# Kernel tuning notes

Hardware: AMD Instinct MI355X
Metric: run time of the kernel (lower is better)

## Reference

```python
import jax, jax.numpy as jnp
import numpy as np

B, N, D_IN, D_OUT = 16, 4096, 256, 128


def setup_inputs() -> dict:
    key = jax.random.key(0)
    ks = jax.random.split(key, 7)
    s_proj = float(np.sqrt(2.0 / D_IN))   # kaiming-ish scale
    s_mlp = float(np.sqrt(2.0 / D_OUT))
    return {
        "X": jax.random.normal(ks[0], (B, N, D_IN), dtype=jnp.float32),
        "W_proj": jax.random.normal(ks[1], (D_IN, D_OUT), dtype=jnp.float32) * s_proj,
        "b_proj": jnp.zeros((D_OUT,), dtype=jnp.float32),
        "W1": jax.random.normal(ks[2], (D_OUT, D_OUT), dtype=jnp.float32) * s_mlp,
        "b1": jnp.zeros((D_OUT,), dtype=jnp.float32),
        "W2": jax.random.normal(ks[3], (D_OUT, D_OUT), dtype=jnp.float32) * s_mlp,
        "b2": jnp.zeros((D_OUT,), dtype=jnp.float32),
    }


def reference(X, W_proj, b_proj, W1, b1, W2, b2):
    # proj: Linear(input_dim, output_dim)
    X = jnp.einsum("bnd,de->bne", X, W_proj) + b_proj
    # mlp: FeedForwardNetwork(D,D,D, num_layers=2) == Linear -> ReLU -> Linear
    X = jax.nn.relu(jnp.einsum("bnd,de->bne", X, W1) + b1)
    X = jnp.einsum("bnd,de->bne", X, W2) + b2
    # leave-one-out sum over the N axis: for each row i, sum of all rows j != i.
    # Identical math to the masked (B,N,N,D) expand-reduce in the torch source.
    return X.sum(axis=1, keepdims=True) - X
```

## Files before the change

kernel.cpp:

```cpp
#include <hip/hip_runtime.h>
#include <stdint.h>

#define D_IN  256
#define D_OUT 128
#define NSEQ  4096
#define NB    16
#define TILE_M 64
#define GRID_M ((NB * NSEQ) / TILE_M)
#define LDS_BYTES 32768

typedef __bf16 bf16x8 __attribute__((ext_vector_type(8)));
typedef float  f32x4  __attribute__((ext_vector_type(4)));

__device__ __forceinline__ unsigned short f2bf(float f) {
  __bf16 h = (__bf16)f;
  union { __bf16 h; unsigned short u; } c; c.h = h;
  return c.u;
}
__device__ __forceinline__ float bf2f(unsigned short u) {
  union { unsigned int u; float f; } a; a.u = ((unsigned int)u) << 16;
  return a.f;
}

__global__ __launch_bounds__(256) void prep(
    const float* __restrict__ Wp, const float* __restrict__ W1, const float* __restrict__ W2,
    const float* __restrict__ bp, const float* __restrict__ b1,
    unsigned short* __restrict__ WaT, unsigned short* __restrict__ W2T, float* __restrict__ be1) {
  int b = blockIdx.x;
  if (b < 128) {
    __shared__ float wp[256];
    int k0 = b * 2;
    wp[threadIdx.x] = Wp[k0 * 128 + threadIdx.x];
    __syncthreads();
    int kk = threadIdx.x >> 7, n = threadIdx.x & 127;
    float s = 0.f;
#pragma unroll 16
    for (int j = 0; j < 128; ++j) s += wp[kk * 128 + j] * W1[j * 128 + n];
    WaT[n * 256 + (k0 + kk)] = f2bf(s);
  } else if (b < 192) {
    int t = (b - 128) * 256 + threadIdx.x;
    int k = t >> 7, n = t & 127;
    W2T[n * 128 + k] = f2bf(W2[t]);
  } else {
    if (threadIdx.x < 128) {
      int n = threadIdx.x;
      float s = b1[n];
#pragma unroll 16
      for (int j = 0; j < 128; ++j) s += bp[j] * W1[j * 128 + n];
      be1[n] = s;
    }
  }
}

template <bool USE_WS>
__global__ __launch_bounds__(256, 3) void fused2(
    const float* __restrict__ X,
    const unsigned short* __restrict__ WaT,
    const unsigned short* __restrict__ W2T,
    const float* __restrict__ be1, const float* __restrict__ b2v,
    unsigned short* __restrict__ Y3, float* __restrict__ out, float* __restrict__ P) {
  extern __shared__ unsigned short smem[];
  unsigned short* bufA = smem;
  unsigned short* bufB = smem + 8192;

  const int tid  = threadIdx.x;
  const int lane = tid & 63;
  const int w    = tid >> 6;
  const int q    = lane >> 4;
  const int l16  = lane & 15;
  const int rowbase = blockIdx.x * TILE_M;
  const int col0 = w * 32 + l16;
  const int col1 = col0 + 16;

  f32x4 acc[4][2];
  bf16x8 bA[4][2], bB[4][2];

#pragma unroll
  for (int ks = 0; ks < 4; ++ks) {
    bA[ks][0] = *(const bf16x8*)(WaT + (size_t)col0 * 256 + ks * 32 + q * 8);
    bA[ks][1] = *(const bf16x8*)(WaT + (size_t)col1 * 256 + ks * 32 + q * 8);
  }

#pragma unroll
  for (int it = 0; it < 8; ++it) {
    int i = tid + it * 256;
    int r = i >> 5, c4 = (i & 31) << 2;
    const float4 v = *(const float4*)(X + (size_t)(rowbase + r) * D_IN + c4);
    ushort4 u; u.x = f2bf(v.x); u.y = f2bf(v.y); u.z = f2bf(v.z); u.w = f2bf(v.w);
    *(ushort4*)(bufA + r * 128 + ((((c4 >> 3) ^ (r & 15)) << 3) + (c4 & 7))) = u;
  }

#pragma unroll
  for (int rt = 0; rt < 4; ++rt) {
    acc[rt][0] = (f32x4){0.f, 0.f, 0.f, 0.f};
    acc[rt][1] = (f32x4){0.f, 0.f, 0.f, 0.f};
  }
  __syncthreads();

  float4 xv[8];
#pragma unroll
  for (int it = 0; it < 8; ++it) {
    int i = tid + it * 256;
    int r = i >> 5, c4 = (i & 31) << 2;
    xv[it] = *(const float4*)(X + (size_t)(rowbase + r) * D_IN + 128 + c4);
  }
#pragma unroll
  for (int ks = 0; ks < 4; ++ks) {
    bB[ks][0] = *(const bf16x8*)(WaT + (size_t)col0 * 256 + 128 + ks * 32 + q * 8);
    bB[ks][1] = *(const bf16x8*)(WaT + (size_t)col1 * 256 + 128 + ks * 32 + q * 8);
  }

#pragma unroll
  for (int ks = 0; ks < 4; ++ks)
#pragma unroll
    for (int rt = 0; rt < 4; ++rt) {
      bf16x8 a = *(const bf16x8*)(bufA + (rt * 16 + l16) * 128 + (((4 * ks + q) ^ l16) << 3));
      acc[rt][0] = __builtin_amdgcn_mfma_f32_16x16x32_bf16(a, bA[ks][0], acc[rt][0], 0, 0, 0);
      acc[rt][1] = __builtin_amdgcn_mfma_f32_16x16x32_bf16(a, bA[ks][1], acc[rt][1], 0, 0, 0);
    }

#pragma unroll
  for (int it = 0; it < 8; ++it) {
    int i = tid + it * 256;
    int r = i >> 5, c4 = (i & 31) << 2;
    ushort4 u; u.x = f2bf(xv[it].x); u.y = f2bf(xv[it].y); u.z = f2bf(xv[it].z); u.w = f2bf(xv[it].w);
    *(ushort4*)(bufB + r * 128 + ((((c4 >> 3) ^ (r & 15)) << 3) + (c4 & 7))) = u;
  }
  __syncthreads();

#pragma unroll
  for (int ks = 0; ks < 4; ++ks) {
    bA[ks][0] = *(const bf16x8*)(W2T + (size_t)col0 * 128 + ks * 32 + q * 8);
    bA[ks][1] = *(const bf16x8*)(W2T + (size_t)col1 * 128 + ks * 32 + q * 8);
  }

#pragma unroll
  for (int ks = 0; ks < 4; ++ks)
#pragma unroll
    for (int rt = 0; rt < 4; ++rt) {
      bf16x8 a = *(const bf16x8*)(bufB + (rt * 16 + l16) * 128 + (((4 * ks + q) ^ l16) << 3));
      acc[rt][0] = __builtin_amdgcn_mfma_f32_16x16x32_bf16(a, bB[ks][0], acc[rt][0], 0, 0, 0);
      acc[rt][1] = __builtin_amdgcn_mfma_f32_16x16x32_bf16(a, bB[ks][1], acc[rt][1], 0, 0, 0);
    }

  {
    const float e0 = be1[col0], e1 = be1[col1];
#pragma unroll
    for (int rt = 0; rt < 4; ++rt)
#pragma unroll
      for (int r = 0; r < 4; ++r) {
        int row = rt * 16 + q * 4 + r;
        int sw = (row & 15) << 3;
        float v0 = acc[rt][0][r] + e0; v0 = v0 > 0.f ? v0 : 0.f;
        float v1 = acc[rt][1][r] + e1; v1 = v1 > 0.f ? v1 : 0.f;
        bufA[row * 128 + ((((col0 >> 3) << 3) ^ sw) + (col0 & 7))] = f2bf(v0);
        bufA[row * 128 + ((((col1 >> 3) << 3) ^ sw) + (col1 & 7))] = f2bf(v1);
      }
  }
  __syncthreads();

#pragma unroll
  for (int rt = 0; rt < 4; ++rt) {
    acc[rt][0] = (f32x4){0.f, 0.f, 0.f, 0.f};
    acc[rt][1] = (f32x4){0.f, 0.f, 0.f, 0.f};
  }
#pragma unroll
  for (int ks = 0; ks < 4; ++ks)
#pragma unroll
    for (int rt = 0; rt < 4; ++rt) {
      bf16x8 a = *(const bf16x8*)(bufA + (rt * 16 + l16) * 128 + (((4 * ks + q) ^ l16) << 3));
      acc[rt][0] = __builtin_amdgcn_mfma_f32_16x16x32_bf16(a, bA[ks][0], acc[rt][0], 0, 0, 0);
      acc[rt][1] = __builtin_amdgcn_mfma_f32_16x16x32_bf16(a, bA[ks][1], acc[rt][1], 0, 0, 0);
    }

  {
    const float bb0 = b2v[col0], bb1 = b2v[col1];
    float s0 = 0.f, s1 = 0.f;
#pragma unroll
    for (int rt = 0; rt < 4; ++rt)
#pragma unroll
      for (int r = 0; r < 4; ++r) {
        int row = rt * 16 + q * 4 + r;
        int sw = (row & 15) << 3;
        float v0 = acc[rt][0][r] + bb0;
        float v1 = acc[rt][1][r] + bb1;
        s0 += v0; s1 += v1;
        bufB[row * 128 + ((((col0 >> 3) << 3) ^ sw) + (col0 & 7))] = f2bf(v0);
        bufB[row * 128 + ((((col1 >> 3) << 3) ^ sw) + (col1 & 7))] = f2bf(v1);
      }
    s0 += __shfl_down(s0, 16); s0 += __shfl_down(s0, 32);
    s1 += __shfl_down(s1, 16); s1 += __shfl_down(s1, 32);
    if (lane < 16) {
      P[(size_t)blockIdx.x * 128 + col0] = s0;
      P[(size_t)blockIdx.x * 128 + col1] = s1;
    }
  }
  __syncthreads();

  if (USE_WS) {
#pragma unroll
    for (int it = 0; it < 4; ++it) {
      int i = tid + it * 256;
      int r = i >> 4, g = i & 15;
      *(uint4*)(Y3 + (size_t)(rowbase + r) * 128 + g * 8) =
          *(const uint4*)(bufB + r * 128 + ((g ^ (r & 15)) << 3));
    }
  } else {
#pragma unroll
    for (int it = 0; it < 8; ++it) {
      int i = tid + it * 256;
      int r = i >> 5, c4 = (i & 31) << 2;
      ushort4 u = *(const ushort4*)(bufB + r * 128 + ((((c4 >> 3) ^ (r & 15)) << 3) + (c4 & 7)));
      float4 v; v.x = bf2f(u.x); v.y = bf2f(u.y); v.z = bf2f(u.z); v.w = bf2f(u.w);
      *(float4*)(out + (size_t)(rowbase + r) * D_OUT + c4) = v;
    }
  }
}

__global__ __launch_bounds__(256) void reduce_S(const float* __restrict__ P, float* __restrict__ S) {
  __shared__ float tmp[128];
  int b = blockIdx.x;
  int col = threadIdx.x & 127;
  int h = threadIdx.x >> 7;
  float s = 0.f;
#pragma unroll
  for (int i = 0; i < 32; ++i) s += P[(size_t)(b * 64 + h * 32 + i) * 128 + col];
  if (h == 1) tmp[col] = s;
  __syncthreads();
  if (h == 0) S[b * 128 + col] = s + tmp[col];
}

__global__ __launch_bounds__(256) void finalize_ws(
    float* __restrict__ out, const unsigned short* __restrict__ Y3, const float* __restrict__ S) {
  size_t g = (size_t)blockIdx.x * 256 + threadIdx.x;
  size_t base = g * 8;
  int row = (int)(base >> 7);
  int col = (int)(base & 127);
  int b = row >> 12;
  uint4 u = *(const uint4*)(Y3 + base);
  float4 s0 = *(const float4*)(S + (b << 7) + col);
  float4 s1 = *(const float4*)(S + (b << 7) + col + 4);
  union { unsigned int uu; float f; } t;
  float4 o0, o1;
  t.uu = u.x << 16;          o0.x = s0.x - t.f;
  t.uu = u.x & 0xFFFF0000u;  o0.y = s0.y - t.f;
  t.uu = u.y << 16;          o0.z = s0.z - t.f;
  t.uu = u.y & 0xFFFF0000u;  o0.w = s0.w - t.f;
  t.uu = u.z << 16;          o1.x = s1.x - t.f;
  t.uu = u.z & 0xFFFF0000u;  o1.y = s1.y - t.f;
  t.uu = u.w << 16;          o1.z = s1.z - t.f;
  t.uu = u.w & 0xFFFF0000u;  o1.w = s1.w - t.f;
  *(float4*)(out + base) = o0;
  *(float4*)(out + base + 4) = o1;
}

__global__ __launch_bounds__(256) void finalize_ip(float* __restrict__ out, const float* __restrict__ S) {
  size_t g = (size_t)blockIdx.x * 256 + threadIdx.x;
  size_t base = g * 8;
  int row = (int)(base >> 7);
  int col = (int)(base & 127);
  int b = row >> 12;
  float4 s0 = *(const float4*)(S + (b << 7) + col);
  float4 s1 = *(const float4*)(S + (b << 7) + col + 4);
  float4 y0 = *(const float4*)(out + base);
  float4 y1 = *(const float4*)(out + base + 4);
  float4 o0, o1;
  o0.x = s0.x - y0.x; o0.y = s0.y - y0.y; o0.z = s0.z - y0.z; o0.w = s0.w - y0.w;
  o1.x = s1.x - y1.x; o1.y = s1.y - y1.y; o1.z = s1.z - y1.z; o1.w = s1.w - y1.w;
  *(float4*)(out + base) = o0;
  *(float4*)(out + base + 4) = o1;
}

extern "C" void kernel_launch(void* const* d_in, const int* in_sizes, int n_in,
                              void* d_out, int out_size, void* d_ws, size_t ws_size,
                              hipStream_t stream) {
  const float* X  = (const float*)d_in[0];
  const float* Wp = (const float*)d_in[1];
  const float* bp = (const float*)d_in[2];
  const float* W1 = (const float*)d_in[3];
  const float* b1 = (const float*)d_in[4];
  const float* W2 = (const float*)d_in[5];
  const float* b2 = (const float*)d_in[6];
  float* out = (float*)d_out;

  char* ws = (char*)d_ws;
  float* S            = (float*)ws;
  float* be1          = (float*)(ws + 8192);
  unsigned short* WaT = (unsigned short*)(ws + 12288);
  unsigned short* W2T = (unsigned short*)(ws + 12288 + 65536);
  float* P            = (float*)(ws + 12288 + 65536 + 32768);
  unsigned short* Y3  = (unsigned short*)(ws + 12288 + 65536 + 32768 + 524288);

  const size_t need = 12288 + 65536 + 32768 + 524288 + (size_t)NB * NSEQ * D_OUT * 2;
  const bool use_ws = ws_size >= need;

  prep<<<193, 256, 0, stream>>>(Wp, W1, W2, bp, b1, WaT, W2T, be1);

  const int fin_blocks = (NB * NSEQ * D_OUT) / (8 * 256);
  if (use_ws) {
    fused2<true><<<GRID_M, 256, LDS_BYTES, stream>>>(X, WaT, W2T, be1, b2, Y3, out, P);
    reduce_S<<<NB, 256, 0, stream>>>(P, S);
    finalize_ws<<<fin_blocks, 256, 0, stream>>>(out, Y3, S);
  } else {
    fused2<false><<<GRID_M, 256, LDS_BYTES, stream>>>(X, WaT, W2T, be1, b2, Y3, out, P);
    reduce_S<<<NB, 256, 0, stream>>>(P, S);
    finalize_ip<<<fin_blocks, 256, 0, stream>>>(out, S);
  }
}
```

Before: 134.3 us.

## Process two row tiles per block and fold S reduction into finalize

The fused kernel now runs 512 blocks that each loop over two 64-row tiles, accumulating the column partial sums across both tiles, which halves the partial-sum buffer. The separate reduce_S launch is removed; each finalize block instead recomputes its batch's column sums from 32 partials into shared memory. This cuts one kernel launch and its dependency gap, at the cost of redundant small reductions in every finalize block and fewer, longer blocks in the main kernel (512 blocks may underfill the GPU's CUs).

```diff
diff --git a/kernel.cpp b/kernel.cpp
--- a/kernel.cpp
+++ b/kernel.cpp
@@ -5,8 +5,7 @@
 #define D_OUT 128
 #define NSEQ  4096
 #define NB    16
-#define TILE_M 64
-#define GRID_M ((NB * NSEQ) / TILE_M)
+#define NBLK  512
 #define LDS_BYTES 32768
 
 typedef __bf16 bf16x8 __attribute__((ext_vector_type(8)));
@@ -68,83 +67,89 @@
   const int w    = tid >> 6;
   const int q    = lane >> 4;
   const int l16  = lane & 15;
-  const int rowbase = blockIdx.x * TILE_M;
+  const int blk  = blockIdx.x;
   const int col0 = w * 32 + l16;
   const int col1 = col0 + 16;
 
+  const float e0  = be1[col0], e1  = be1[col1];
+  const float bb0 = b2v[col0], bb1 = b2v[col1];
+
   f32x4 acc[4][2];
   bf16x8 bA[4][2], bB[4][2];
-
-#pragma unroll
-  for (int ks = 0; ks < 4; ++ks) {
-    bA[ks][0] = *(const bf16x8*)(WaT + (size_t)col0 * 256 + ks * 32 + q * 8);
-    bA[ks][1] = *(const bf16x8*)(WaT + (size_t)col1 * 256 + ks * 32 + q * 8);
-  }
-
-#pragma unroll
-  for (int it = 0; it < 8; ++it) {
-    int i = tid + it * 256;
-    int r = i >> 5, c4 = (i & 31) << 2;
-    const float4 v = *(const float4*)(X + (size_t)(rowbase + r) * D_IN + c4);
-    ushort4 u; u.x = f2bf(v.x); u.y = f2bf(v.y); u.z = f2bf(v.z); u.w = f2bf(v.w);
-    *(ushort4*)(bufA + r * 128 + ((((c4 >> 3) ^ (r & 15)) << 3) + (c4 & 7))) = u;
-  }
-
-#pragma unroll
-  for (int rt = 0; rt < 4; ++rt) {
-    acc[rt][0] = (f32x4){0.f, 0.f, 0.f, 0.f};
-    acc[rt][1] = (f32x4){0.f, 0.f, 0.f, 0.f};
-  }
-  __syncthreads();
-
-  float4 xv[8];
-#pragma unroll
-  for (int it = 0; it < 8; ++it) {
-    int i = tid + it * 256;
-    int r = i >> 5, c4 = (i & 31) << 2;
-    xv[it] = *(const float4*)(X + (size_t)(rowbase + r) * D_IN + 128 + c4);
-  }
-#pragma unroll
-  for (int ks = 0; ks < 4; ++ks) {
-    bB[ks][0] = *(const bf16x8*)(WaT + (size_t)col0 * 256 + 128 + ks * 32 + q * 8);
-    bB[ks][1] = *(const bf16x8*)(WaT + (size_t)col1 * 256 + 128 + ks * 32 + q * 8);
-  }
-
-#pragma unroll
-  for (int ks = 0; ks < 4; ++ks)
+  float s0 = 0.f, s1 = 0.f;
+
+#pragma unroll 1
+  for (int t = 0; t < 2; ++t) {
+    const int rowbase = blk * 128 + t * 64;
+
+#pragma unroll
+    for (int ks = 0; ks < 4; ++ks) {
+      bA[ks][0] = *(const bf16x8*)(WaT + (size_t)col0 * 256 + ks * 32 + q * 8);
+      bA[ks][1] = *(const bf16x8*)(WaT + (size_t)col1 * 256 + ks * 32 + q * 8);
+    }
+
+#pragma unroll
+    for (int it = 0; it < 8; ++it) {
+      int i = tid + it * 256;
+      int r = i >> 5, c4 = (i & 31) << 2;
+      const float4 v = *(const float4*)(X + (size_t)(rowbase + r) * D_IN + c4);
+      ushort4 u; u.x = f2bf(v.x); u.y = f2bf(v.y); u.z = f2bf(v.z); u.w = f2bf(v.w);
+      *(ushort4*)(bufA + r * 128 + ((((c4 >> 3) ^ (r & 15)) << 3) + (c4 & 7))) = u;
+    }
+
 #pragma unroll
     for (int rt = 0; rt < 4; ++rt) {
-      bf16x8 a = *(const bf16x8*)(bufA + (rt * 16 + l16) * 128 + (((4 * ks + q) ^ l16) << 3));
-      acc[rt][0] = __builtin_amdgcn_mfma_f32_16x16x32_bf16(a, bA[ks][0], acc[rt][0], 0, 0, 0);
-      acc[rt][1] = __builtin_amdgcn_mfma_f32_16x16x32_bf16(a, bA[ks][1], acc[rt][1], 0, 0, 0);
-    }
-
-#pragma unroll
-  for (int it = 0; it < 8; ++it) {
-    int i = tid + it * 256;
-    int r = i >> 5, c4 = (i & 31) << 2;
-    ushort4 u; u.x = f2bf(xv[it].x); u.y = f2bf(xv[it].y); u.z = f2bf(xv[it].z); u.w = f2bf(xv[it].w);
-    *(ushort4*)(bufB + r * 128 + ((((c4 >> 3) ^ (r & 15)) << 3) + (c4 & 7))) = u;
-  }
-  __syncthreads();
-
-#pragma unroll
-  for (int ks = 0; ks < 4; ++ks) {
-    bA[ks][0] = *(const bf16x8*)(W2T + (size_t)col0 * 128 + ks * 32 + q * 8);
-    bA[ks][1] = *(const bf16x8*)(W2T + (size_t)col1 * 128 + ks * 32 + q * 8);
-  }
-
-#pragma unroll
-  for (int ks = 0; ks < 4; ++ks)
-#pragma unroll
-    for (int rt = 0; rt < 4; ++rt) {
-      bf16x8 a = *(const bf16x8*)(bufB + (rt * 16 + l16) * 128 + (((4 * ks + q) ^ l16) << 3));
-      acc[rt][0] = __builtin_amdgcn_mfma_f32_16x16x32_bf16(a, bB[ks][0], acc[rt][0], 0, 0, 0);
-      acc[rt][1] = __builtin_amdgcn_mfma_f32_16x16x32_bf16(a, bB[ks][1], acc[rt][1], 0, 0, 0);
-    }
-
-  {
-    const float e0 = be1[col0], e1 = be1[col1];
+      acc[rt][0] = (f32x4){0.f, 0.f, 0.f, 0.f};
+      acc[rt][1] = (f32x4){0.f, 0.f, 0.f, 0.f};
+    }
+    __syncthreads();
+
+    float4 xv[8];
+#pragma unroll
+    for (int it = 0; it < 8; ++it) {
+      int i = tid + it * 256;
+      int r = i >> 5, c4 = (i & 31) << 2;
+      xv[it] = *(const float4*)(X + (size_t)(rowbase + r) * D_IN + 128 + c4);
+    }
+#pragma unroll
+    for (int ks = 0; ks < 4; ++ks) {
+      bB[ks][0] = *(const bf16x8*)(WaT + (size_t)col0 * 256 + 128 + ks * 32 + q * 8);
+      bB[ks][1] = *(const bf16x8*)(WaT + (size_t)col1 * 256 + 128 + ks * 32 + q * 8);
+    }
+
+#pragma unroll
+    for (int ks = 0; ks < 4; ++ks)
+#pragma unroll
+      for (int rt = 0; rt < 4; ++rt) {
+        bf16x8 a = *(const bf16x8*)(bufA + (rt * 16 + l16) * 128 + (((4 * ks + q) ^ l16) << 3));
+        acc[rt][0] = __builtin_amdgcn_mfma_f32_16x16x32_bf16(a, bA[ks][0], acc[rt][0], 0, 0, 0);
+        acc[rt][1] = __builtin_amdgcn_mfma_f32_16x16x32_bf16(a, bA[ks][1], acc[rt][1], 0, 0, 0);
+      }
+
+#pragma unroll
+    for (int it = 0; it < 8; ++it) {
+      int i = tid + it * 256;
+      int r = i >> 5, c4 = (i & 31) << 2;
+      ushort4 u; u.x = f2bf(xv[it].x); u.y = f2bf(xv[it].y); u.z = f2bf(xv[it].z); u.w = f2bf(xv[it].w);
+      *(ushort4*)(bufB + r * 128 + ((((c4 >> 3) ^ (r & 15)) << 3) + (c4 & 7))) = u;
+    }
+    __syncthreads();
+
+#pragma unroll
+    for (int ks = 0; ks < 4; ++ks) {
+      bA[ks][0] = *(const bf16x8*)(W2T + (size_t)col0 * 128 + ks * 32 + q * 8);
+      bA[ks][1] = *(const bf16x8*)(W2T + (size_t)col1 * 128 + ks * 32 + q * 8);
+    }
+
+#pragma unroll
+    for (int ks = 0; ks < 4; ++ks)
+#pragma unroll
+      for (int rt = 0; rt < 4; ++rt) {
+        bf16x8 a = *(const bf16x8*)(bufB + (rt * 16 + l16) * 128 + (((4 * ks + q) ^ l16) << 3));
+        acc[rt][0] = __builtin_amdgcn_mfma_f32_16x16x32_bf16(a, bB[ks][0], acc[rt][0], 0, 0, 0);
+        acc[rt][1] = __builtin_amdgcn_mfma_f32_16x16x32_bf16(a, bB[ks][1], acc[rt][1], 0, 0, 0);
+      }
+
 #pragma unroll
     for (int rt = 0; rt < 4; ++rt)
 #pragma unroll
@@ -156,26 +161,22 @@
         bufA[row * 128 + ((((col0 >> 3) << 3) ^ sw) + (col0 & 7))] = f2bf(v0);
         bufA[row * 128 + ((((col1 >> 3) << 3) ^ sw) + (col1 & 7))] = f2bf(v1);
       }
-  }
-  __syncthreads();
-
-#pragma unroll
-  for (int rt = 0; rt < 4; ++rt) {
-    acc[rt][0] = (f32x4){0.f, 0.f, 0.f, 0.f};
-    acc[rt][1] = (f32x4){0.f, 0.f, 0.f, 0.f};
-  }
-#pragma unroll
-  for (int ks = 0; ks < 4; ++ks)
+    __syncthreads();
+
 #pragma unroll
     for (int rt = 0; rt < 4; ++rt) {
-      bf16x8 a = *(const bf16x8*)(bufA + (rt * 16 + l16) * 128 + (((4 * ks + q) ^ l16) << 3));
-      acc[rt][0] = __builtin_amdgcn_mfma_f32_16x16x32_bf16(a, bA[ks][0], acc[rt][0], 0, 0, 0);
-      acc[rt][1] = __builtin_amdgcn_mfma_f32_16x16x32_bf16(a, bA[ks][1], acc[rt][1], 0, 0, 0);
-    }
-
-  {
-    const float bb0 = b2v[col0], bb1 = b2v[col1];
-    float s0 = 0.f, s1 = 0.f;
+      acc[rt][0] = (f32x4){0.f, 0.f, 0.f, 0.f};
+      acc[rt][1] = (f32x4){0.f, 0.f, 0.f, 0.f};
+    }
+#pragma unroll
+    for (int ks = 0; ks < 4; ++ks)
+#pragma unroll
+      for (int rt = 0; rt < 4; ++rt) {
+        bf16x8 a = *(const bf16x8*)(bufA + (rt * 16 + l16) * 128 + (((4 * ks + q) ^ l16) << 3));
+        acc[rt][0] = __builtin_amdgcn_mfma_f32_16x16x32_bf16(a, bA[ks][0], acc[rt][0], 0, 0, 0);
+        acc[rt][1] = __builtin_amdgcn_mfma_f32_16x16x32_bf16(a, bA[ks][1], acc[rt][1], 0, 0, 0);
+      }
+
 #pragma unroll
     for (int rt = 0; rt < 4; ++rt)
 #pragma unroll
@@ -188,58 +189,55 @@
         bufB[row * 128 + ((((col0 >> 3) << 3) ^ sw) + (col0 & 7))] = f2bf(v0);
         bufB[row * 128 + ((((col1 >> 3) << 3) ^ sw) + (col1 & 7))] = f2bf(v1);
       }
-    s0 += __shfl_down(s0, 16); s0 += __shfl_down(s0, 32);
-    s1 += __shfl_down(s1, 16); s1 += __shfl_down(s1, 32);
-    if (lane < 16) {
-      P[(size_t)blockIdx.x * 128 + col0] = s0;
-      P[(size_t)blockIdx.x * 128 + col1] = s1;
-    }
+    __syncthreads();
+
+    if (USE_WS) {
+#pragma unroll
+      for (int it = 0; it < 4; ++it) {
+        int i = tid + it * 256;
+        int r = i >> 4, g = i & 15;
+        *(uint4*)(Y3 + (size_t)(rowbase + r) * 128 + g * 8) =
+            *(const uint4*)(bufB + r * 128 + ((g ^ (r & 15)) << 3));
+      }
+    } else {
+#pragma unroll
+      for (int it = 0; it < 8; ++it) {
+        int i = tid + it * 256;
+        int r = i >> 5, c4 = (i & 31) << 2;
+        ushort4 u = *(const ushort4*)(bufB + r * 128 + ((((c4 >> 3) ^ (r & 15)) << 3) + (c4 & 7)));
+        float4 v; v.x = bf2f(u.x); v.y = bf2f(u.y); v.z = bf2f(u.z); v.w = bf2f(u.w);
+        *(float4*)(out + (size_t)(rowbase + r) * D_OUT + c4) = v;
+      }
+    }
+  }
+
+  s0 += __shfl_down(s0, 16); s0 += __shfl_down(s0, 32);
+  s1 += __shfl_down(s1, 16); s1 += __shfl_down(s1, 32);
+  if (lane < 16) {
+    P[(size_t)blk * 128 + col0] = s0;
+    P[(size_t)blk * 128 + col1] = s1;
+  }
+}
+
+__global__ __launch_bounds__(256) void finalize_ws(
+    float* __restrict__ out, const unsigned short* __restrict__ Y3, const float* __restrict__ P) {
+  __shared__ float S[128];
+  const int tid  = threadIdx.x;
+  const int row0 = blockIdx.x * 16;
+  const int b    = row0 >> 12;
+  if (tid < 128) {
+    float s = 0.f;
+    const float* p = P + (size_t)b * 32 * 128 + tid;
+#pragma unroll
+    for (int i = 0; i < 32; ++i) s += p[i * 128];
+    S[tid] = s;
   }
   __syncthreads();
-
-  if (USE_WS) {
-#pragma unroll
-    for (int it = 0; it < 4; ++it) {
-      int i = tid + it * 256;
-      int r = i >> 4, g = i & 15;
-      *(uint4*)(Y3 + (size_t)(rowbase + r) * 128 + g * 8) =
-          *(const uint4*)(bufB + r * 128 + ((g ^ (r & 15)) << 3));
-    }
-  } else {
-#pragma unroll
-    for (int it = 0; it < 8; ++it) {
-      int i = tid + it * 256;
-      int r = i >> 5, c4 = (i & 31) << 2;
-      ushort4 u = *(const ushort4*)(bufB + r * 128 + ((((c4 >> 3) ^ (r & 15)) << 3) + (c4 & 7)));
-      float4 v; v.x = bf2f(u.x); v.y = bf2f(u.y); v.z = bf2f(u.z); v.w = bf2f(u.w);
-      *(float4*)(out + (size_t)(rowbase + r) * D_OUT + c4) = v;
-    }
-  }
-}
-
-__global__ __launch_bounds__(256) void reduce_S(const float* __restrict__ P, float* __restrict__ S) {
-  __shared__ float tmp[128];
-  int b = blockIdx.x;
-  int col = threadIdx.x & 127;
-  int h = threadIdx.x >> 7;
-  float s = 0.f;
-#pragma unroll
-  for (int i = 0; i < 32; ++i) s += P[(size_t)(b * 64 + h * 32 + i) * 128 + col];
-  if (h == 1) tmp[col] = s;
-  __syncthreads();
-  if (h == 0) S[b * 128 + col] = s + tmp[col];
-}
-
-__global__ __launch_bounds__(256) void finalize_ws(
-    float* __restrict__ out, const unsigned short* __restrict__ Y3, const float* __restrict__ S) {
-  size_t g = (size_t)blockIdx.x * 256 + threadIdx.x;
-  size_t base = g * 8;
-  int row = (int)(base >> 7);
-  int col = (int)(base & 127);
-  int b = row >> 12;
+  size_t base = (size_t)row0 * 128 + (size_t)tid * 8;
+  int col = (tid * 8) & 127;
   uint4 u = *(const uint4*)(Y3 + base);
-  float4 s0 = *(const float4*)(S + (b << 7) + col);
-  float4 s1 = *(const float4*)(S + (b << 7) + col + 4);
+  float4 s0 = *(const float4*)(S + col);
+  float4 s1 = *(const float4*)(S + col + 4);
   union { unsigned int uu; float f; } t;
   float4 o0, o1;
   t.uu = u.x << 16;          o0.x = s0.x - t.f;
@@ -254,14 +252,24 @@
   *(float4*)(out + base + 4) = o1;
 }
 
-__global__ __launch_bounds__(256) void finalize_ip(float* __restrict__ out, const float* __restrict__ S) {
-  size_t g = (size_t)blockIdx.x * 256 + threadIdx.x;
-  size_t base = g * 8;
-  int row = (int)(base >> 7);
-  int col = (int)(base & 127);
-  int b = row >> 12;
-  float4 s0 = *(const float4*)(S + (b << 7) + col);
-  float4 s1 = *(const float4*)(S + (b << 7) + col + 4);
+__global__ __launch_bounds__(256) void finalize_ip(
+    float* __restrict__ out, const float* __restrict__ P) {
+  __shared__ float S[128];
+  const int tid  = threadIdx.x;
+  const int row0 = blockIdx.x * 16;
+  const int b    = row0 >> 12;
+  if (tid < 128) {
+    float s = 0.f;
+    const float* p = P + (size_t)b * 32 * 128 + tid;
+#pragma unroll
+    for (int i = 0; i < 32; ++i) s += p[i * 128];
+    S[tid] = s;
+  }
+  __syncthreads();
+  size_t base = (size_t)row0 * 128 + (size_t)tid * 8;
+  int col = (tid * 8) & 127;
+  float4 s0 = *(const float4*)(S + col);
+  float4 s1 = *(const float4*)(S + col + 4);
   float4 y0 = *(const float4*)(out + base);
   float4 y1 = *(const float4*)(out + base + 4);
   float4 o0, o1;
@@ -284,26 +292,23 @@
   float* out = (float*)d_out;
 
   char* ws = (char*)d_ws;
-  float* S            = (float*)ws;
-  float* be1          = (float*)(ws + 8192);
-  unsigned short* WaT = (unsigned short*)(ws + 12288);
-  unsigned short* W2T = (unsigned short*)(ws + 12288 + 65536);
-  float* P            = (float*)(ws + 12288 + 65536 + 32768);
-  unsigned short* Y3  = (unsigned short*)(ws + 12288 + 65536 + 32768 + 524288);
-
-  const size_t need = 12288 + 65536 + 32768 + 524288 + (size_t)NB * NSEQ * D_OUT * 2;
+  float* be1          = (float*)ws;
+  unsigned short* WaT = (unsigned short*)(ws + 4096);
+  unsigned short* W2T = (unsigned short*)(ws + 4096 + 65536);
+  float* P            = (float*)(ws + 4096 + 65536 + 32768);
+  unsigned short* Y3  = (unsigned short*)(ws + 4096 + 65536 + 32768 + 262144);
+
+  const size_t need = 4096 + 65536 + 32768 + 262144 + (size_t)NB * NSEQ * D_OUT * 2;
   const bool use_ws = ws_size >= need;
 
   prep<<<193, 256, 0, stream>>>(Wp, W1, W2, bp, b1, WaT, W2T, be1);
 
-  const int fin_blocks = (NB * NSEQ * D_OUT) / (8 * 256);
+  const int fin_blocks = (NB * NSEQ) / 16;
   if (use_ws) {
-    fused2<true><<<GRID_M, 256, LDS_BYTES, stream>>>(X, WaT, W2T, be1, b2, Y3, out, P);
-    reduce_S<<<NB, 256, 0, stream>>>(P, S);
-    finalize_ws<<<fin_blocks, 256, 0, stream>>>(out, Y3, S);
+    fused2<true><<<NBLK, 256, LDS_BYTES, stream>>>(X, WaT, W2T, be1, b2, Y3, out, P);
+    finalize_ws<<<fin_blocks, 256, 0, stream>>>(out, Y3, P);
   } else {
-    fused2<false><<<GRID_M, 256, LDS_BYTES, stream>>>(X, WaT, W2T, be1, b2, Y3, out, P);
-    reduce_S<<<NB, 256, 0, stream>>>(P, S);
-    finalize_ip<<<fin_blocks, 256, 0, stream>>>(out, S);
-  }
-}
+    fused2<false><<<NBLK, 256, LDS_BYTES, stream>>>(X, WaT, W2T, be1, b2, Y3, out, P);
+    finalize_ip<<<fin_blocks, 256, 0, stream>>>(out, P);
+  }
+}
```

New measurement: 172.4 us. 1.28x slower.
